# Kernel tuning notes

Measured on AMD Instinct MI355X. Metric: run time of the kernel, lower is better.

The kernel has to match this reference:

```python
import jax, jax.numpy as jnp
import numpy as np

SUB = 5      # icosphere subdivisions -> V = 10*4^5 + 2 = 10242
B = 16       # batch size
ZD = 32      # z_dim
HID = 64     # hidden_dim


def _create_icosphere(sub):
    t = (1.0 + np.sqrt(5.0)) / 2.0
    v = np.array([[-1, t, 0], [1, t, 0], [-1, -t, 0], [1, -t, 0], [0, -1, t], [0, 1, t],
                  [0, -1, -t], [0, 1, -t], [t, 0, -1], [t, 0, 1], [-t, 0, -1], [-t, 0, 1]],
                 dtype=np.float32)
    v /= np.linalg.norm(v[0])
    f = np.array([[0, 11, 5], [0, 5, 1], [0, 1, 7], [0, 7, 10], [0, 10, 11], [1, 5, 9],
                  [5, 11, 4], [11, 10, 2], [10, 7, 6], [7, 1, 8], [3, 9, 4], [3, 4, 2],
                  [3, 2, 6], [3, 6, 8], [3, 8, 9], [4, 9, 5], [2, 4, 11], [6, 2, 10],
                  [8, 6, 7], [9, 8, 1]], dtype=np.int64)
    for _ in range(sub):
        mid = {}
        nv = list(v)
        nf = []
        def gm(i1, i2):
            k = (min(i1, i2), max(i1, i2))
            if k not in mid:
                m = (v[i1] + v[i2]) / 2.0
                m = m / np.linalg.norm(m)
                mid[k] = len(nv)
                nv.append(m)
            return mid[k]
        for v0, v1, v2 in f:
            a, b, c = gm(v0, v1), gm(v1, v2), gm(v2, v0)
            nf.extend([[v0, a, c], [v1, b, a], [v2, c, b], [a, b, c]])
        v = np.array(nv, dtype=np.float32)
        f = np.array(nf, dtype=np.int64)
    return v, f


def _adjacency(faces, nv):
    # symmetric edges + self loops, sym-normalized: 1/sqrt(deg[r]*deg[c])
    e = set()
    for a, b, c in faces:
        e.update([(int(a), int(b)), (int(b), int(a)), (int(b), int(c)),
                  (int(c), int(b)), (int(c), int(a)), (int(a), int(c))])
    for i in range(nv):
        e.add((i, i))
    e = np.array(sorted(e), dtype=np.int64)
    row, col = e[:, 0], e[:, 1]
    deg = np.bincount(row, minlength=nv).astype(np.float32)
    vals = (1.0 / np.sqrt(deg[row] * deg[col])).astype(np.float32)
    return row.astype(np.int32), col.astype(np.int32), vals


def _lin(key, din, dout):
    W = jax.random.normal(key, (dout, din), jnp.float32) / np.sqrt(din)
    b = jnp.zeros((dout,), jnp.float32)
    return W, b


def setup_inputs() -> dict:
    verts, faces = _create_icosphere(SUB)
    V = len(verts)
    row, col, vals = _adjacency(faces, V)
    template = jnp.asarray(verts)

    key = jax.random.key(0)
    ks = jax.random.split(key, 16)
    # input meshes = template + small deformation (realistic for this VAE)
    x = template[None] + 0.05 * jax.random.normal(ks[0], (B, V, 3), jnp.float32)
    eps = jax.random.normal(ks[1], (B, ZD), jnp.float32)

    W1, b1 = _lin(ks[2], 3, HID)
    W2, b2 = _lin(ks[3], HID, HID)
    W3, b3 = _lin(ks[4], HID, 2 * HID)
    Wfc, bfc = _lin(ks[5], 2 * HID, 4 * HID)
    Wmu, bmu = _lin(ks[6], 4 * HID, ZD)
    Wlv, blv = _lin(ks[7], 4 * HID, ZD)
    DH = 2 * HID  # decoder hidden_dim = 128
    Wd1, bd1 = _lin(ks[8], ZD + 3, DH)
    Wd2, bd2 = _lin(ks[9], DH, DH)
    Wd3, bd3 = _lin(ks[10], DH, DH // 2)
    Wd4, bd4 = _lin(ks[11], DH // 2, 3)

    return {"x": x, "eps": eps, "row": jnp.asarray(row), "col": jnp.asarray(col),
            "vals": jnp.asarray(vals), "template": template,
            "W1": W1, "b1": b1, "W2": W2, "b2": b2, "W3": W3, "b3": b3,
            "Wfc": Wfc, "bfc": bfc, "Wmu": Wmu, "bmu": bmu, "Wlv": Wlv, "blv": blv,
            "Wd1": Wd1, "bd1": bd1, "Wd2": Wd2, "bd2": bd2,
            "Wd3": Wd3, "bd3": bd3, "Wd4": Wd4, "bd4": bd4}


def _spmm(row, col, vals, h):
    # batched sparse (V,V) @ (B,V,C): out[b,r] = sum_e vals[e] * h[b, col[e]]
    msg = h[:, col, :] * vals[None, :, None]            # (B, E, C)
    return jnp.zeros(h.shape, h.dtype).at[:, row, :].add(msg)


def _linear(x, W, b):
    return x @ W.T + b


def reference(x, eps, row, col, vals, template,
              W1, b1, W2, b2, W3, b3, Wfc, bfc, Wmu, bmu, Wlv, blv,
              Wd1, bd1, Wd2, bd2, Wd3, bd3, Wd4, bd4):
    # --- encoder: 3 graph convs (linear -> spmm -> relu), mean pool, fc ---
    h = jax.nn.relu(_spmm(row, col, vals, _linear(x, W1, b1)))
    h = jax.nn.relu(_spmm(row, col, vals, _linear(h, W2, b2)))
    h = jax.nn.relu(_spmm(row, col, vals, _linear(h, W3, b3)))
    g = h.mean(axis=1)                                   # (B, 2*HID)
    feat = jax.nn.relu(_linear(g, Wfc, bfc))             # (B, 4*HID)
    mu = _linear(feat, Wmu, bmu)                         # (B, ZD)
    log_var = jnp.clip(_linear(feat, Wlv, blv), -20.0, 20.0)
    # --- reparameterize (eps supplied as input for determinism) ---
    z = mu + eps * jnp.exp(0.5 * log_var)
    # --- decoder MLP on [z, template] per vertex (dropout = eval mode) ---
    Bn, V = x.shape[0], template.shape[0]
    z_exp = jnp.broadcast_to(z[:, None, :], (Bn, V, z.shape[-1]))
    t_exp = jnp.broadcast_to(template[None], (Bn, V, 3))
    hd = jnp.concatenate([z_exp, t_exp], axis=-1)        # (B, V, ZD+3)
    hd = jax.nn.relu(_linear(hd, Wd1, bd1))
    hd = jax.nn.relu(_linear(hd, Wd2, bd2))
    hd = jax.nn.relu(_linear(hd, Wd3, bd3))
    offsets = _linear(hd, Wd4, bd4)                      # (B, V, 3)
    recon = template[None] + offsets
    return recon, mu, log_var
```

## Files before the change

kernel.cpp:

```cpp
#include <hip/hip_runtime.h>
#include <hip/hip_bf16.h>

typedef __attribute__((ext_vector_type(8))) unsigned short ushort8;
typedef __attribute__((ext_vector_type(4))) unsigned short ushort4v;
typedef __attribute__((ext_vector_type(8))) short short8v;
typedef __attribute__((ext_vector_type(4))) float f32x4;

__device__ __forceinline__ float bf2f(unsigned short u){
  union { unsigned int i; float f; } x; x.i = ((unsigned int)u) << 16; return x.f;
}
__device__ __forceinline__ unsigned short f2bf(float f){
  __hip_bfloat16 h = __float2bfloat16(f);
  return *reinterpret_cast<unsigned short*>(&h);
}

__device__ __forceinline__ void sw_decode(int p, int NB, int& b, int& off){
  int xcd = p & 7, q = p >> 3;
  int hi = (q >= NB) ? 1 : 0;
  b = xcd + (hi << 3);
  off = q - (hi ? NB : 0);
}

__global__ void prep_k(const int* __restrict__ row, const int* __restrict__ colx,
                       const float* __restrict__ vals, int nnz,
                       int* __restrict__ col7, float* __restrict__ val7,
                       float* __restrict__ dvec, float* __restrict__ g, int V, int GN){
  int v = blockIdx.x*256 + threadIdx.x;
  if (v < GN) g[v] = 0.f;
  if (v >= V) return;
  int lo = 0, hi = nnz;
  while (lo < hi){ int m = (lo+hi)>>1; if (row[m] < v) lo = m+1; else hi = m; }
  int e0 = lo;
  int lo2 = e0; hi = nnz;
  while (lo2 < hi){ int m = (lo2+hi)>>1; if (row[m] < v+1) lo2 = m+1; else hi = m; }
  int e1 = lo2;
  float s = 0.f;
  #pragma unroll
  for (int i=0;i<7;i++){
    int e = e0 + i;
    int c  = (e < e1) ? colx[e] : 0;
    float wv = (e < e1) ? vals[e] : 0.f;
    col7[v*7+i] = c; val7[v*7+i] = wv; s += wv;
  }
  dvec[v] = s;
}

__global__ void spmm_lin1_k(const float* __restrict__ x, const int* __restrict__ col7,
    const float* __restrict__ val7, const float* __restrict__ d,
    const float* __restrict__ W1, const float* __restrict__ b1,
    unsigned short* __restrict__ out, int V, int NB){
  __shared__ float sW[192];
  __shared__ float sB[64];
  int tid = threadIdx.x;
  if (tid < 192) sW[tid] = W1[tid];
  if (tid < 64)  sB[tid] = b1[tid];
  __syncthreads();
  int b, off; sw_decode(blockIdx.x, NB, b, off);
  int v = off*256 + tid;
  if (v >= V) return;
  const float* xb = x + (size_t)b*V*3;
  int   cs[7]; float ws[7];
  #pragma unroll
  for (int i=0;i<7;i++){ cs[i] = col7[v*7+i]; ws[i] = val7[v*7+i]; }
  float s0=0.f, s1=0.f, s2=0.f;
  #pragma unroll
  for (int i=0;i<7;i++){
    const float* xr = xb + (size_t)cs[i]*3;
    s0 += ws[i]*xr[0]; s1 += ws[i]*xr[1]; s2 += ws[i]*xr[2];
  }
  float dv = d[v];
  unsigned short* orow = out + ((size_t)b*V + v)*64;
  #pragma unroll
  for (int cg=0; cg<8; ++cg){
    ushort8 o;
    #pragma unroll
    for (int k=0;k<8;k++){
      int c = cg*8 + k;
      float acc = dv*sB[c] + s0*sW[c*3] + s1*sW[c*3+1] + s2*sW[c*3+2];
      o[k] = f2bf(fmaxf(acc, 0.f));
    }
    *reinterpret_cast<ushort8*>(orow + cg*8) = o;
  }
}

__global__ __launch_bounds__(256) void spmm8s_k(const unsigned short* __restrict__ in,
    unsigned short* __restrict__ out, const int* __restrict__ col7,
    const float* __restrict__ val7, int V, int NB){
  int b, off; sw_decode(blockIdx.x, NB, b, off);
  int j = off*256 + (int)threadIdx.x;
  if (j >= V*8) return;
  int cg = j & 7; int v = j >> 3;
  const unsigned short* base = in + (size_t)b*V*64 + cg*8;
  int cols[7]; float vv[7];
  #pragma unroll
  for (int i=0;i<7;i++){ cols[i] = col7[v*7+i]; vv[i] = val7[v*7+i]; }
  ushort8 g[7];
  #pragma unroll
  for (int i=0;i<7;i++) g[i] = *reinterpret_cast<const ushort8*>(base + (size_t)cols[i]*64);
  float acc[8];
  #pragma unroll
  for (int k=0;k<8;k++) acc[k] = 0.f;
  #pragma unroll
  for (int i=0;i<7;i++){
    float s = vv[i];
    #pragma unroll
    for (int k=0;k<8;k++) acc[k] += s*bf2f(g[i][k]);
  }
  ushort8 o;
  #pragma unroll
  for (int k=0;k<8;k++) o[k] = f2bf(acc[k]);
  *reinterpret_cast<ushort8*>(out + ((size_t)b*V + v)*64 + cg*8) = o;
}

template<int K, int N, bool RELU>
__global__ __launch_bounds__(256) void lin_mfma_k(const unsigned short* __restrict__ in,
    const float* __restrict__ W, const float* __restrict__ bias,
    unsigned short* __restrict__ out, const float* __restrict__ dvec, int V, int NB){
  constexpr int KP = K + 8;
  constexpr int NF = N / 16;
  constexpr int KS = K / 32;
  __shared__ unsigned short sW[N * KP];
  __shared__ float sB[N];
  int tid = threadIdx.x;
  for (int i = tid*4; i < N*K; i += 1024){
    const float4 wv = *reinterpret_cast<const float4*>(W + i);
    int n = i / K, k = i - n*K;
    unsigned short* dst = &sW[n*KP + k];
    dst[0] = f2bf(wv.x); dst[1] = f2bf(wv.y); dst[2] = f2bf(wv.z); dst[3] = f2bf(wv.w);
  }
  if (tid < N) sB[tid] = bias[tid];
  __syncthreads();

  int b, off; sw_decode(blockIdx.x, NB, b, off);
  const int wave = tid >> 6, lane = tid & 63;
  const int l15 = lane & 15, lg = lane >> 4;
  const int vbase = off*128 + wave*32;

  int v0r = vbase + l15, v1r = vbase + 16 + l15;
  int v0c = min(v0r, V-1), v1c = min(v1r, V-1);
  const size_t bb = (size_t)b*V;
  const unsigned short* bp0 = in + (bb + v0c)*K + lg*8;
  const unsigned short* bp1 = in + (bb + v1c)*K + lg*8;
  const unsigned short* aBase = &sW[l15*KP + lg*8];

  f32x4 acc[NF][2];
  #pragma unroll
  for (int nf=0; nf<NF; ++nf){ acc[nf][0] = (f32x4)0.f; acc[nf][1] = (f32x4)0.f; }

  #pragma unroll
  for (int ks=0; ks<KS; ++ks){
    short8v b0 = *reinterpret_cast<const short8v*>(bp0 + ks*32);
    short8v b1 = *reinterpret_cast<const short8v*>(bp1 + ks*32);
    #pragma unroll
    for (int nf=0; nf<NF; ++nf){
      short8v a = *reinterpret_cast<const short8v*>(aBase + nf*16*KP + ks*32);
      acc[nf][0] = __builtin_amdgcn_mfma_f32_16x16x32_bf16(a, b0, acc[nf][0], 0,0,0);
      acc[nf][1] = __builtin_amdgcn_mfma_f32_16x16x32_bf16(a, b1, acc[nf][1], 0,0,0);
    }
  }

  float d0 = dvec[v0c], d1 = dvec[v1c];
  #pragma unroll
  for (int rr=0; rr<2; ++rr){
    int v = rr ? v1r : v0r;
    if (v >= V) continue;
    float ds = rr ? d1 : d0;
    #pragma unroll
    for (int nf=0; nf<NF; ++nf){
      int nb = nf*16 + lg*4;
      ushort4v o;
      #pragma unroll
      for (int reg=0; reg<4; ++reg){
        float val = acc[nf][rr][reg] + ds*sB[nb + reg];
        if (RELU) val = val > 0.f ? val : 0.f;
        o[reg] = f2bf(val);
      }
      *reinterpret_cast<ushort4v*>(out + (bb + v)*N + nb) = o;
    }
  }
}

__global__ __launch_bounds__(256) void lin3_mean_k(const unsigned short* __restrict__ in,
    const float* __restrict__ W, const float* __restrict__ bias,
    const float* __restrict__ dvec, float* __restrict__ g, int V, int NB){
  constexpr int K = 64, N = 128, KP = K + 8, NF = N/16, KS = K/32;
  __shared__ unsigned short sW[N * KP];
  __shared__ float sB[N];
  __shared__ float gPart[128];
  int tid = threadIdx.x;
  for (int i = tid*4; i < N*K; i += 1024){
    const float4 wv = *reinterpret_cast<const float4*>(W + i);
    int n = i / K, k = i - n*K;
    unsigned short* dst = &sW[n*KP + k];
    dst[0] = f2bf(wv.x); dst[1] = f2bf(wv.y); dst[2] = f2bf(wv.z); dst[3] = f2bf(wv.w);
  }
  if (tid < N) sB[tid] = bias[tid];
  if (tid < 128) gPart[tid] = 0.f;
  __syncthreads();

  int b, off; sw_decode(blockIdx.x, NB, b, off);
  const int wave = tid >> 6, lane = tid & 63;
  const int l15 = lane & 15, lg = lane >> 4;
  const int vbase = off*128 + wave*32;

  int v0r = vbase + l15, v1r = vbase + 16 + l15;
  int v0c = min(v0r, V-1), v1c = min(v1r, V-1);
  const size_t bb = (size_t)b*V;
  const unsigned short* bp0 = in + (bb + v0c)*K + lg*8;
  const unsigned short* bp1 = in + (bb + v1c)*K + lg*8;
  const unsigned short* aBase = &sW[l15*KP + lg*8];

  f32x4 acc[NF][2];
  #pragma unroll
  for (int nf=0; nf<NF; ++nf){ acc[nf][0] = (f32x4)0.f; acc[nf][1] = (f32x4)0.f; }

  #pragma unroll
  for (int ks=0; ks<KS; ++ks){
    short8v b0 = *reinterpret_cast<const short8v*>(bp0 + ks*32);
    short8v b1 = *reinterpret_cast<const short8v*>(bp1 + ks*32);
    #pragma unroll
    for (int nf=0; nf<NF; ++nf){
      short8v a = *reinterpret_cast<const short8v*>(aBase + nf*16*KP + ks*32);
      acc[nf][0] = __builtin_amdgcn_mfma_f32_16x16x32_bf16(a, b0, acc[nf][0], 0,0,0);
      acc[nf][1] = __builtin_amdgcn_mfma_f32_16x16x32_bf16(a, b1, acc[nf][1], 0,0,0);
    }
  }

  bool ok0 = v0r < V, ok1 = v1r < V;
  float d0 = dvec[v0c], d1 = dvec[v1c];
  #pragma unroll
  for (int nf=0; nf<NF; ++nf){
    #pragma unroll
    for (int reg=0; reg<4; ++reg){
      int c = nf*16 + lg*4 + reg;
      float v0f = fmaxf(acc[nf][0][reg] + d0*sB[c], 0.f);
      float v1f = fmaxf(acc[nf][1][reg] + d1*sB[c], 0.f);
      float sA = (ok0 ? v0f : 0.f) + (ok1 ? v1f : 0.f);
      #pragma unroll
      for (int m=1; m<16; m<<=1) sA += __shfl_xor(sA, m);
      if (l15 == 0) atomicAdd(&gPart[c], sA);
    }
  }
  __syncthreads();
  if (tid < 128){
    float a = gPart[tid];
    if (a != 0.f) atomicAdd(&g[b*128 + tid], a);
  }
}

__global__ __launch_bounds__(256) void head2_k(const float* __restrict__ g,
    const float* __restrict__ Wfc, const float* __restrict__ bfc,
    const float* __restrict__ Wmu, const float* __restrict__ bmu,
    const float* __restrict__ Wlv, const float* __restrict__ blv,
    const float* __restrict__ eps, const float* __restrict__ Wd1,
    const float* __restrict__ bd1, float* __restrict__ mu_out,
    float* __restrict__ lv_out, float* __restrict__ zp, float invV){
  int b = blockIdx.x;
  int tid = threadIdx.x;
  __shared__ float sG[128];
  __shared__ float sF[256];
  __shared__ float sMu[32];
  __shared__ float sLv[32];
  __shared__ float sZ[32];
  if (tid < 128) sG[tid] = g[b*128 + tid] * invV;
  __syncthreads();
  {
    const float4* wr = reinterpret_cast<const float4*>(Wfc + tid*128);
    float acc = bfc[tid];
    #pragma unroll 8
    for (int k4=0;k4<32;k4++){
      float4 wv = wr[k4];
      acc += sG[k4*4]*wv.x + sG[k4*4+1]*wv.y + sG[k4*4+2]*wv.z + sG[k4*4+3]*wv.w;
    }
    sF[tid] = fmaxf(acc, 0.f);
  }
  __syncthreads();
  if (tid < 64){
    int c = tid & 31;
    bool isMu = tid < 32;
    const float4* wr = reinterpret_cast<const float4*>((isMu ? Wmu : Wlv) + c*256);
    float acc = isMu ? bmu[c] : blv[c];
    #pragma unroll 8
    for (int k4=0;k4<64;k4++){
      float4 wv = wr[k4];
      acc += sF[k4*4]*wv.x + sF[k4*4+1]*wv.y + sF[k4*4+2]*wv.z + sF[k4*4+3]*wv.w;
    }
    if (isMu){ sMu[c] = acc; mu_out[b*32+c] = acc; }
    else {
      acc = fminf(20.f, fmaxf(-20.f, acc));
      sLv[c] = acc; lv_out[b*32+c] = acc;
    }
  }
  __syncthreads();
  if (tid < 32) sZ[tid] = sMu[tid] + eps[b*32+tid]*expf(0.5f*sLv[tid]);
  __syncthreads();
  if (tid < 128){
    const float* wr = Wd1 + tid*35;
    float acc = bd1[tid];
    #pragma unroll
    for (int k=0;k<32;k++) acc += sZ[k]*wr[k];
    zp[b*128 + tid] = acc;
  }
}

__global__ __launch_bounds__(256) void dec_k(const float* __restrict__ zp,
    const float* __restrict__ tmpl, const float* __restrict__ Wd1,
    const float* __restrict__ Wd2, const float* __restrict__ bd2,
    const float* __restrict__ Wd3, const float* __restrict__ bd3,
    const float* __restrict__ Wd4, const float* __restrict__ bd4,
    float* __restrict__ out, int V, int NB){
  constexpr int KP = 152;
  __shared__ unsigned short sW[64*KP];
  __shared__ unsigned short sH[128*KP];
  __shared__ float sB2[128];
  __shared__ float sB3[64];
  __shared__ float sW4[192];
  __shared__ float sB4[3];
  __shared__ float sZPb[128];
  __shared__ float sWT[128*3];
  int tid = threadIdx.x;
  int b, off; sw_decode(blockIdx.x, NB, b, off);

  if (tid < 128) sB2[tid] = bd2[tid];
  if (tid < 64)  sB3[tid] = bd3[tid];
  if (tid < 192) sW4[tid] = Wd4[tid];
  if (tid < 3)   sB4[tid] = bd4[tid];
  if (tid < 128) sZPb[tid] = zp[b*128 + tid];
  if (tid < 128){
    sWT[tid*3+0] = Wd1[tid*35+32];
    sWT[tid*3+1] = Wd1[tid*35+33];
    sWT[tid*3+2] = Wd1[tid*35+34];
  }
  auto stageW = [&](const float* Wsrc){
    for (int i = tid*4; i < 64*128; i += 1024){
      float4 wv = *reinterpret_cast<const float4*>(Wsrc + i);
      int n = i >> 7, k = i & 127;
      unsigned short* dst = &sW[n*KP + k];
      dst[0]=f2bf(wv.x); dst[1]=f2bf(wv.y); dst[2]=f2bf(wv.z); dst[3]=f2bf(wv.w);
    }
  };
  stageW(Wd2);
  __syncthreads();

  const int wave = tid >> 6, lane = tid & 63;
  const int l15 = lane & 15, lg = lane >> 4;
  const int vbase = off*128 + wave*32;
  const int lrow = wave*32;

  int v0r = vbase + l15, v1r = vbase + 16 + l15;
  int v0 = min(v0r, V-1), v1 = min(v1r, V-1);
  float t0x=tmpl[v0*3], t0y=tmpl[v0*3+1], t0z=tmpl[v0*3+2];
  float t1x=tmpl[v1*3], t1y=tmpl[v1*3+1], t1z=tmpl[v1*3+2];

  short8v bf0[4], bf1[4];
  #pragma unroll
  for (int ks=0; ks<4; ++ks){
    #pragma unroll
    for (int k=0;k<8;k++){
      int c = lg*8 + ks*32 + k;
      const float* wt = &sWT[c*3];
      float zc = sZPb[c];
      bf0[ks][k] = (short)f2bf(fmaxf(zc + t0x*wt[0]+t0y*wt[1]+t0z*wt[2], 0.f));
      bf1[ks][k] = (short)f2bf(fmaxf(zc + t1x*wt[0]+t1y*wt[1]+t1z*wt[2], 0.f));
    }
  }

  const unsigned short* aBase = &sW[l15*KP + lg*8];

  #pragma unroll
  for (int half=0; half<2; ++half){
    if (half==1){
      __syncthreads();
      stageW(Wd2 + 64*128);
      __syncthreads();
    }
    f32x4 acc[4][2];
    #pragma unroll
    for (int nf=0; nf<4; ++nf){ acc[nf][0]=(f32x4)0.f; acc[nf][1]=(f32x4)0.f; }
    #pragma unroll
    for (int ks=0; ks<4; ++ks){
      #pragma unroll
      for (int nf=0; nf<4; ++nf){
        short8v a = *reinterpret_cast<const short8v*>(aBase + nf*16*KP + ks*32);
        acc[nf][0] = __builtin_amdgcn_mfma_f32_16x16x32_bf16(a, bf0[ks], acc[nf][0], 0,0,0);
        acc[nf][1] = __builtin_amdgcn_mfma_f32_16x16x32_bf16(a, bf1[ks], acc[nf][1], 0,0,0);
      }
    }
    #pragma unroll
    for (int rr=0; rr<2; ++rr){
      #pragma unroll
      for (int nf=0; nf<4; ++nf){
        int c = half*64 + nf*16 + lg*4;
        ushort4v o;
        #pragma unroll
        for (int reg=0; reg<4; ++reg)
          o[reg] = f2bf(fmaxf(acc[nf][rr][reg] + sB2[c+reg], 0.f));
        *reinterpret_cast<ushort4v*>(&sH[(lrow + rr*16 + l15)*KP + c]) = o;
      }
    }
  }
  __syncthreads();
  stageW(Wd3);
  __syncthreads();

  f32x4 acc3[4][2];
  #pragma unroll
  for (int nf=0; nf<4; ++nf){ acc3[nf][0]=(f32x4)0.f; acc3[nf][1]=(f32x4)0.f; }
  #pragma unroll
  for (int ks=0; ks<4; ++ks){
    short8v h0 = *reinterpret_cast<const short8v*>(&sH[(lrow + l15)*KP + ks*32 + lg*8]);
    short8v h1 = *reinterpret_cast<const short8v*>(&sH[(lrow + 16 + l15)*KP + ks*32 + lg*8]);
    #pragma unroll
    for (int nf=0; nf<4; ++nf){
      short8v a = *reinterpret_cast<const short8v*>(aBase + nf*16*KP + ks*32);
      acc3[nf][0] = __builtin_amdgcn_mfma_f32_16x16x32_bf16(a, h0, acc3[nf][0], 0,0,0);
      acc3[nf][1] = __builtin_amdgcn_mfma_f32_16x16x32_bf16(a, h1, acc3[nf][1], 0,0,0);
    }
  }

  #pragma unroll
  for (int rr=0; rr<2; ++rr){
    int vr = rr ? v1r : v0r;
    float p0 = 0.f, p1 = 0.f, p2 = 0.f;
    #pragma unroll
    for (int nf=0; nf<4; ++nf){
      #pragma unroll
      for (int reg=0; reg<4; ++reg){
        int c = nf*16 + lg*4 + reg;
        float h = fmaxf(acc3[nf][rr][reg] + sB3[c], 0.f);
        p0 += h*sW4[c]; p1 += h*sW4[64+c]; p2 += h*sW4[128+c];
      }
    }
    p0 += __shfl_xor(p0,16); p0 += __shfl_xor(p0,32);
    p1 += __shfl_xor(p1,16); p1 += __shfl_xor(p1,32);
    p2 += __shfl_xor(p2,16); p2 += __shfl_xor(p2,32);
    if (lg == 0 && vr < V){
      size_t o = ((size_t)b*V + vr)*3;
      out[o+0] = tmpl[vr*3+0] + p0 + sB4[0];
      out[o+1] = tmpl[vr*3+1] + p1 + sB4[1];
      out[o+2] = tmpl[vr*3+2] + p2 + sB4[2];
    }
  }
}

extern "C" void kernel_launch(void* const* d_in, const int* in_sizes, int n_in,
                              void* d_out, int out_size, void* d_ws, size_t ws_size,
                              hipStream_t stream){
  const float* x    = (const float*)d_in[0];
  const float* eps  = (const float*)d_in[1];
  const int*   row  = (const int*)d_in[2];
  const int*   colx = (const int*)d_in[3];
  const float* vals = (const float*)d_in[4];
  const float* tmpl = (const float*)d_in[5];
  const float* W1 = (const float*)d_in[6];  const float* b1 = (const float*)d_in[7];
  const float* W2 = (const float*)d_in[8];  const float* b2 = (const float*)d_in[9];
  const float* W3 = (const float*)d_in[10]; const float* b3 = (const float*)d_in[11];
  const float* Wfc= (const float*)d_in[12]; const float* bfc= (const float*)d_in[13];
  const float* Wmu= (const float*)d_in[14]; const float* bmu= (const float*)d_in[15];
  const float* Wlv= (const float*)d_in[16]; const float* blv= (const float*)d_in[17];
  const float* Wd1= (const float*)d_in[18]; const float* bd1= (const float*)d_in[19];
  const float* Wd2= (const float*)d_in[20]; const float* bd2= (const float*)d_in[21];
  const float* Wd3= (const float*)d_in[22]; const float* bd3= (const float*)d_in[23];
  const float* Wd4= (const float*)d_in[24]; const float* bd4= (const float*)d_in[25];

  int V   = in_sizes[5] / 3;
  int Bn  = in_sizes[1] / 32;
  int nnz = in_sizes[2];
  int R   = Bn * V;

  char* w = (char*)d_ws;
  size_t off = 0;
  auto alloc = [&](size_t bytes)->char*{
    char* p = w + off; off = (off + bytes + 255) & ~(size_t)255; return p;
  };
  unsigned short* bufA = (unsigned short*)alloc((size_t)R * 64 * 2);
  unsigned short* bufB = (unsigned short*)alloc((size_t)R * 64 * 2);
  int*   col7 = (int*)alloc((size_t)V*7*4);
  float* val7 = (float*)alloc((size_t)V*7*4);
  float* dvec = (float*)alloc((size_t)V*4);
  float* g    = (float*)alloc((size_t)Bn*128*4);
  float* zpb  = (float*)alloc((size_t)Bn*128*4);

  float* recon  = (float*)d_out;
  float* mu_out = recon + (size_t)R*3;
  float* lv_out = mu_out + (size_t)Bn*32;

  int NB1 = (V + 255) / 256;
  int NB8 = (V*8 + 255) / 256;
  int NBm = (V + 127) / 128;

  prep_k<<<(V+255)/256, 256, 0, stream>>>(row, colx, vals, nnz, col7, val7, dvec, g, V, Bn*128);

  spmm_lin1_k<<<16*NB1, 256, 0, stream>>>(x, col7, val7, dvec, W1, b1, bufA, V, NB1);
  spmm8s_k<<<16*NB8, 256, 0, stream>>>(bufA, bufB, col7, val7, V, NB8);
  lin_mfma_k<64,64,true><<<16*NBm, 256, 0, stream>>>(bufB, W2, b2, bufA, dvec, V, NBm);
  spmm8s_k<<<16*NB8, 256, 0, stream>>>(bufA, bufB, col7, val7, V, NB8);
  lin3_mean_k<<<16*NBm, 256, 0, stream>>>(bufB, W3, b3, dvec, g, V, NBm);

  head2_k<<<Bn, 256, 0, stream>>>(g, Wfc, bfc, Wmu, bmu, Wlv, blv, eps, Wd1, bd1,
                                  mu_out, lv_out, zpb, 1.0f/(float)V);

  dec_k<<<16*NBm, 256, 0, stream>>>(zpb, tmpl, Wd1, Wd2, bd2, Wd3, bd3, Wd4, bd4,
                                    recon, V, NBm);
}
```

Measured before the change: 131.9 us.

## Pad neighbor lists to 8 for vector loads; halve decoder tile per block

Neighbor column and value arrays are padded from 7 to 8 entries per vertex so each thread loads them with 16-byte vector loads instead of scalar loads. The decoder kernel now handles 64 vertices per block (16 per wave) instead of 128. It uses a smaller LDS padding stride and half the hidden-state buffer, which lowers LDS and register use and doubles the grid size. The trade-off is that each block stages the Wd2/Wd3 weights for fewer vertices, so the weight conversion and staging work is repeated across twice as many blocks.

Measured after the change: 132.2 us. About the same (+0.2%).

```diff
diff --git a/kernel.cpp b/kernel.cpp
--- a/kernel.cpp
+++ b/kernel.cpp
@@ -23,7 +23,7 @@
 
 __global__ void prep_k(const int* __restrict__ row, const int* __restrict__ colx,
                        const float* __restrict__ vals, int nnz,
-                       int* __restrict__ col7, float* __restrict__ val7,
+                       int* __restrict__ col8, float* __restrict__ val8,
                        float* __restrict__ dvec, float* __restrict__ g, int V, int GN){
   int v = blockIdx.x*256 + threadIdx.x;
   if (v < GN) g[v] = 0.f;
@@ -36,17 +36,29 @@
   int e1 = lo2;
   float s = 0.f;
   #pragma unroll
-  for (int i=0;i<7;i++){
+  for (int i=0;i<8;i++){
     int e = e0 + i;
     int c  = (e < e1) ? colx[e] : 0;
     float wv = (e < e1) ? vals[e] : 0.f;
-    col7[v*7+i] = c; val7[v*7+i] = wv; s += wv;
+    col8[v*8+i] = c; val8[v*8+i] = wv; s += wv;
   }
   dvec[v] = s;
 }
 
-__global__ void spmm_lin1_k(const float* __restrict__ x, const int* __restrict__ col7,
-    const float* __restrict__ val7, const float* __restrict__ d,
+__device__ __forceinline__ void load_nbr(const int* __restrict__ col8,
+    const float* __restrict__ val8, int v, int* cols, float* vv){
+  int4 ca = *reinterpret_cast<const int4*>(col8 + v*8);
+  int4 cb = *reinterpret_cast<const int4*>(col8 + v*8 + 4);
+  float4 va = *reinterpret_cast<const float4*>(val8 + v*8);
+  float4 vb = *reinterpret_cast<const float4*>(val8 + v*8 + 4);
+  cols[0]=ca.x; cols[1]=ca.y; cols[2]=ca.z; cols[3]=ca.w;
+  cols[4]=cb.x; cols[5]=cb.y; cols[6]=cb.z;
+  vv[0]=va.x; vv[1]=va.y; vv[2]=va.z; vv[3]=va.w;
+  vv[4]=vb.x; vv[5]=vb.y; vv[6]=vb.z;
+}
+
+__global__ void spmm_lin1_k(const float* __restrict__ x, const int* __restrict__ col8,
+    const float* __restrict__ val8, const float* __restrict__ d,
     const float* __restrict__ W1, const float* __restrict__ b1,
     unsigned short* __restrict__ out, int V, int NB){
   __shared__ float sW[192];
@@ -60,8 +72,7 @@
   if (v >= V) return;
   const float* xb = x + (size_t)b*V*3;
   int   cs[7]; float ws[7];
-  #pragma unroll
-  for (int i=0;i<7;i++){ cs[i] = col7[v*7+i]; ws[i] = val7[v*7+i]; }
+  load_nbr(col8, val8, v, cs, ws);
   float s0=0.f, s1=0.f, s2=0.f;
   #pragma unroll
   for (int i=0;i<7;i++){
@@ -84,16 +95,15 @@
 }
 
 __global__ __launch_bounds__(256) void spmm8s_k(const unsigned short* __restrict__ in,
-    unsigned short* __restrict__ out, const int* __restrict__ col7,
-    const float* __restrict__ val7, int V, int NB){
+    unsigned short* __restrict__ out, const int* __restrict__ col8,
+    const float* __restrict__ val8, int V, int NB){
   int b, off; sw_decode(blockIdx.x, NB, b, off);
   int j = off*256 + (int)threadIdx.x;
   if (j >= V*8) return;
   int cg = j & 7; int v = j >> 3;
   const unsigned short* base = in + (size_t)b*V*64 + cg*8;
   int cols[7]; float vv[7];
-  #pragma unroll
-  for (int i=0;i<7;i++){ cols[i] = col7[v*7+i]; vv[i] = val7[v*7+i]; }
+  load_nbr(col8, val8, v, cols, vv);
   ushort8 g[7];
   #pragma unroll
   for (int i=0;i<7;i++) g[i] = *reinterpret_cast<const ushort8*>(base + (size_t)cols[i]*64);
@@ -309,9 +319,9 @@
     const float* __restrict__ Wd3, const float* __restrict__ bd3,
     const float* __restrict__ Wd4, const float* __restrict__ bd4,
     float* __restrict__ out, int V, int NB){
-  constexpr int KP = 152;
+  constexpr int KP = 136;
   __shared__ unsigned short sW[64*KP];
-  __shared__ unsigned short sH[128*KP];
+  __shared__ unsigned short sH[64*KP];
   __shared__ float sB2[128];
   __shared__ float sB3[64];
   __shared__ float sW4[192];
@@ -344,24 +354,21 @@
 
   const int wave = tid >> 6, lane = tid & 63;
   const int l15 = lane & 15, lg = lane >> 4;
-  const int vbase = off*128 + wave*32;
-  const int lrow = wave*32;
-
-  int v0r = vbase + l15, v1r = vbase + 16 + l15;
-  int v0 = min(v0r, V-1), v1 = min(v1r, V-1);
+  const int vbase = off*64 + wave*16;
+  const int lrow = wave*16;
+
+  int v0r = vbase + l15;
+  int v0 = min(v0r, V-1);
   float t0x=tmpl[v0*3], t0y=tmpl[v0*3+1], t0z=tmpl[v0*3+2];
-  float t1x=tmpl[v1*3], t1y=tmpl[v1*3+1], t1z=tmpl[v1*3+2];
-
-  short8v bf0[4], bf1[4];
+
+  short8v bf0[4];
   #pragma unroll
   for (int ks=0; ks<4; ++ks){
     #pragma unroll
     for (int k=0;k<8;k++){
       int c = lg*8 + ks*32 + k;
       const float* wt = &sWT[c*3];
-      float zc = sZPb[c];
-      bf0[ks][k] = (short)f2bf(fmaxf(zc + t0x*wt[0]+t0y*wt[1]+t0z*wt[2], 0.f));
-      bf1[ks][k] = (short)f2bf(fmaxf(zc + t1x*wt[0]+t1y*wt[1]+t1z*wt[2], 0.f));
+      bf0[ks][k] = (short)f2bf(fmaxf(sZPb[c] + t0x*wt[0]+t0y*wt[1]+t0z*wt[2], 0.f));
     }
   }
 
@@ -374,72 +381,62 @@
       stageW(Wd2 + 64*128);
       __syncthreads();
     }
-    f32x4 acc[4][2];
-    #pragma unroll
-    for (int nf=0; nf<4; ++nf){ acc[nf][0]=(f32x4)0.f; acc[nf][1]=(f32x4)0.f; }
+    f32x4 acc[4];
+    #pragma unroll
+    for (int nf=0; nf<4; ++nf) acc[nf]=(f32x4)0.f;
     #pragma unroll
     for (int ks=0; ks<4; ++ks){
       #pragma unroll
       for (int nf=0; nf<4; ++nf){
         short8v a = *reinterpret_cast<const short8v*>(aBase + nf*16*KP + ks*32);
-        acc[nf][0] = __builtin_amdgcn_mfma_f32_16x16x32_bf16(a, bf0[ks], acc[nf][0], 0,0,0);
-        acc[nf][1] = __builtin_amdgcn_mfma_f32_16x16x32_bf16(a, bf1[ks], acc[nf][1], 0,0,0);
+        acc[nf] = __builtin_amdgcn_mfma_f32_16x16x32_bf16(a, bf0[ks], acc[nf], 0,0,0);
       }
     }
     #pragma unroll
-    for (int rr=0; rr<2; ++rr){
+    for (int nf=0; nf<4; ++nf){
+      int c = half*64 + nf*16 + lg*4;
+      ushort4v o;
       #pragma unroll
-      for (int nf=0; nf<4; ++nf){
-        int c = half*64 + nf*16 + lg*4;
-        ushort4v o;
-        #pragma unroll
-        for (int reg=0; reg<4; ++reg)
-          o[reg] = f2bf(fmaxf(acc[nf][rr][reg] + sB2[c+reg], 0.f));
-        *reinterpret_cast<ushort4v*>(&sH[(lrow + rr*16 + l15)*KP + c]) = o;
-      }
+      for (int reg=0; reg<4; ++reg)
+        o[reg] = f2bf(fmaxf(acc[nf][reg] + sB2[c+reg], 0.f));
+      *reinterpret_cast<ushort4v*>(&sH[(lrow + l15)*KP + c]) = o;
     }
   }
   __syncthreads();
   stageW(Wd3);
   __syncthreads();
 
-  f32x4 acc3[4][2];
-  #pragma unroll
-  for (int nf=0; nf<4; ++nf){ acc3[nf][0]=(f32x4)0.f; acc3[nf][1]=(f32x4)0.f; }
+  f32x4 acc3[4];
+  #pragma unroll
+  for (int nf=0; nf<4; ++nf) acc3[nf]=(f32x4)0.f;
   #pragma unroll
   for (int ks=0; ks<4; ++ks){
     short8v h0 = *reinterpret_cast<const short8v*>(&sH[(lrow + l15)*KP + ks*32 + lg*8]);
-    short8v h1 = *reinterpret_cast<const short8v*>(&sH[(lrow + 16 + l15)*KP + ks*32 + lg*8]);
     #pragma unroll
     for (int nf=0; nf<4; ++nf){
       short8v a = *reinterpret_cast<const short8v*>(aBase + nf*16*KP + ks*32);
-      acc3[nf][0] = __builtin_amdgcn_mfma_f32_16x16x32_bf16(a, h0, acc3[nf][0], 0,0,0);
-      acc3[nf][1] = __builtin_amdgcn_mfma_f32_16x16x32_bf16(a, h1, acc3[nf][1], 0,0,0);
-    }
-  }
-
-  #pragma unroll
-  for (int rr=0; rr<2; ++rr){
-    int vr = rr ? v1r : v0r;
-    float p0 = 0.f, p1 = 0.f, p2 = 0.f;
-    #pragma unroll
-    for (int nf=0; nf<4; ++nf){
-      #pragma unroll
-      for (int reg=0; reg<4; ++reg){
-        int c = nf*16 + lg*4 + reg;
-        float h = fmaxf(acc3[nf][rr][reg] + sB3[c], 0.f);
-        p0 += h*sW4[c]; p1 += h*sW4[64+c]; p2 += h*sW4[128+c];
-      }
-    }
-    p0 += __shfl_xor(p0,16); p0 += __shfl_xor(p0,32);
-    p1 += __shfl_xor(p1,16); p1 += __shfl_xor(p1,32);
-    p2 += __shfl_xor(p2,16); p2 += __shfl_xor(p2,32);
-    if (lg == 0 && vr < V){
-      size_t o = ((size_t)b*V + vr)*3;
-      out[o+0] = tmpl[vr*3+0] + p0 + sB4[0];
-      out[o+1] = tmpl[vr*3+1] + p1 + sB4[1];
-      out[o+2] = tmpl[vr*3+2] + p2 + sB4[2];
-    }
+      acc3[nf] = __builtin_amdgcn_mfma_f32_16x16x32_bf16(a, h0, acc3[nf], 0,0,0);
+    }
+  }
+
+  float p0 = 0.f, p1 = 0.f, p2 = 0.f;
+  #pragma unroll
+  for (int nf=0; nf<4; ++nf){
+    #pragma unroll
+    for (int reg=0; reg<4; ++reg){
+      int c = nf*16 + lg*4 + reg;
+      float h = fmaxf(acc3[nf][reg] + sB3[c], 0.f);
+      p0 += h*sW4[c]; p1 += h*sW4[64+c]; p2 += h*sW4[128+c];
+    }
+  }
+  p0 += __shfl_xor(p0,16); p0 += __shfl_xor(p0,32);
+  p1 += __shfl_xor(p1,16); p1 += __shfl_xor(p1,32);
+  p2 += __shfl_xor(p2,16); p2 += __shfl_xor(p2,32);
+  if (lg == 0 && v0r < V){
+    size_t o = ((size_t)b*V + v0r)*3;
+    out[o+0] = tmpl[v0r*3+0] + p0 + sB4[0];
+    out[o+1] = tmpl[v0r*3+1] + p1 + sB4[1];
+    out[o+2] = tmpl[v0r*3+2] + p2 + sB4[2];
   }
 }
 
@@ -475,8 +472,8 @@
   };
   unsigned short* bufA = (unsigned short*)alloc((size_t)R * 64 * 2);
   unsigned short* bufB = (unsigned short*)alloc((size_t)R * 64 * 2);
-  int*   col7 = (int*)alloc((size_t)V*7*4);
-  float* val7 = (float*)alloc((size_t)V*7*4);
+  int*   col8 = (int*)alloc((size_t)V*8*4);
+  float* val8 = (float*)alloc((size_t)V*8*4);
   float* dvec = (float*)alloc((size_t)V*4);
   float* g    = (float*)alloc((size_t)Bn*128*4);
   float* zpb  = (float*)alloc((size_t)Bn*128*4);
@@ -488,18 +485,19 @@
   int NB1 = (V + 255) / 256;
   int NB8 = (V*8 + 255) / 256;
   int NBm = (V + 127) / 128;
-
-  prep_k<<<(V+255)/256, 256, 0, stream>>>(row, colx, vals, nnz, col7, val7, dvec, g, V, Bn*128);
-
-  spmm_lin1_k<<<16*NB1, 256, 0, stream>>>(x, col7, val7, dvec, W1, b1, bufA, V, NB1);
-  spmm8s_k<<<16*NB8, 256, 0, stream>>>(bufA, bufB, col7, val7, V, NB8);
+  int NBd = (V + 63) / 64;
+
+  prep_k<<<(V+255)/256, 256, 0, stream>>>(row, colx, vals, nnz, col8, val8, dvec, g, V, Bn*128);
+
+  spmm_lin1_k<<<16*NB1, 256, 0, stream>>>(x, col8, val8, dvec, W1, b1, bufA, V, NB1);
+  spmm8s_k<<<16*NB8, 256, 0, stream>>>(bufA, bufB, col8, val8, V, NB8);
   lin_mfma_k<64,64,true><<<16*NBm, 256, 0, stream>>>(bufB, W2, b2, bufA, dvec, V, NBm);
-  spmm8s_k<<<16*NB8, 256, 0, stream>>>(bufA, bufB, col7, val7, V, NB8);
+  spmm8s_k<<<16*NB8, 256, 0, stream>>>(bufA, bufB, col8, val8, V, NB8);
   lin3_mean_k<<<16*NBm, 256, 0, stream>>>(bufB, W3, b3, dvec, g, V, NBm);
 
   head2_k<<<Bn, 256, 0, stream>>>(g, Wfc, bfc, Wmu, bmu, Wlv, blv, eps, Wd1, bd1,
                                   mu_out, lv_out, zpb, 1.0f/(float)V);
 
-  dec_k<<<16*NBm, 256, 0, stream>>>(zpb, tmpl, Wd1, Wd2, bd2, Wd3, bd3, Wd4, bd4,
-                                    recon, V, NBm);
-}
+  dec_k<<<16*NBd, 256, 0, stream>>>(zpb, tmpl, Wd1, Wd2, bd2, Wd3, bd3, Wd4, bd4,
+                                    recon, V, NBd);
+}
```
